# Kernel optimization log

Hardware: AMD Instinct MI355X
Metric: run time of the kernel (lower is better)

Reference implementation:

```python
import jax, jax.numpy as jnp
import numpy as np

N, E, S, G = 524288, 2097152, 8192, 64
F_IN, HID = 64, 128


def setup_inputs() -> dict:
    key = jax.random.key(0)
    ks = jax.random.split(key, 12)
    x = jax.random.normal(ks[0], (N, F_IN), dtype=jnp.float32)
    edge_index = jax.random.randint(ks[1], (2, E), 0, N, dtype=jnp.int64)
    node_batch = jnp.sort(jax.random.randint(ks[2], (N,), 0, S, dtype=jnp.int64))
    weights = jax.random.uniform(ks[3], (S, 1), dtype=jnp.float32)
    subgraph_batch = jnp.sort(jax.random.randint(ks[4], (S,), 0, G, dtype=jnp.int64))
    s = 1.0 / np.sqrt(F_IN)
    h = 1.0 / np.sqrt(HID)
    W_l = jax.random.uniform(ks[5], (F_IN, HID), jnp.float32, -s, s)
    W_r = jax.random.uniform(ks[6], (F_IN, HID), jnp.float32, -s, s)
    b_conv = jax.random.uniform(ks[7], (HID,), jnp.float32, -s, s)
    W1 = jax.random.uniform(ks[8], (HID, HID), jnp.float32, -h, h)
    b1 = jax.random.uniform(ks[9], (HID,), jnp.float32, -h, h)
    W2 = jax.random.uniform(ks[10], (HID, 1), jnp.float32, -h, h)
    b2 = jax.random.uniform(ks[11], (1,), jnp.float32, -h, h)
    return {"x": x, "edge_index": edge_index, "node_batch": node_batch,
            "weights": weights, "subgraph_batch": subgraph_batch,
            "W_l": W_l, "W_r": W_r, "b_conv": b_conv,
            "W1": W1, "b1": b1, "W2": W2, "b2": b2}


def reference(x, edge_index, node_batch, weights, subgraph_batch,
              W_l, W_r, b_conv, W1, b1, W2, b2):
    src, dst = edge_index[0], edge_index[1]
    # GraphSAGE mean aggregation: gather neighbor feats, scatter-mean to dst
    msg_sum = jax.ops.segment_sum(x[src], dst, num_segments=N)  # [N, F_IN]
    deg = jax.ops.segment_sum(jnp.ones((E,), x.dtype), dst, num_segments=N)
    agg = msg_sum / jnp.maximum(deg, 1.0)[:, None]
    h = jax.nn.relu(agg @ W_l + x @ W_r + b_conv)               # [N, HID]
    # global_add_pool nodes -> subgraph embeddings
    g = jax.ops.segment_sum(h, node_batch, num_segments=S)      # [S, HID]
    # MLP head -> scalar per subgraph
    s = jax.nn.leaky_relu(g @ W1 + b1, negative_slope=0.01) @ W2 + b2  # [S, 1]
    sw = s * weights
    energy = jax.ops.segment_sum(sw, subgraph_batch, num_segments=G)   # [G, 1]
    norm = jax.ops.segment_sum(weights, subgraph_batch, num_segments=G)
    return energy / norm
```

## Files before the change

### kernel.cpp

```cpp
#include <hip/hip_runtime.h>
#include <hip/hip_bf16.h>

#define NN 524288
#define NE 2097152
#define NS 8192
#define NG 64
#define FIN 64
#define HIDDEN 128

#define NB 512
#define BIN_NODES 1024
#define CAP 4608

typedef __attribute__((ext_vector_type(8))) unsigned short ushort8;
typedef __attribute__((ext_vector_type(8))) short bf16x8;
typedef __attribute__((ext_vector_type(4))) float floatx4;

__device__ __forceinline__ unsigned short f2b(float f) {
  union { float f; unsigned int u; } c; c.f = f;
  unsigned int u = c.u;
  unsigned int r = (u + 0x7FFFu + ((u >> 16) & 1u)) >> 16;
  return (unsigned short)r;
}
__device__ __forceinline__ float b2f(unsigned short b) {
  union { unsigned int u; float f; } c; c.u = ((unsigned int)b) << 16;
  return c.f;
}

__global__ __launch_bounds__(256) void k_cast(const float* __restrict__ x,
                                              unsigned short* __restrict__ xb) {
  size_t i = ((size_t)blockIdx.x * 256 + threadIdx.x) * 8;
  float4 v0 = *(const float4*)(x + i);
  float4 v1 = *(const float4*)(x + i + 4);
  ushort8 r;
  r[0] = f2b(v0.x); r[1] = f2b(v0.y); r[2] = f2b(v0.z); r[3] = f2b(v0.w);
  r[4] = f2b(v1.x); r[5] = f2b(v1.y); r[6] = f2b(v1.z); r[7] = f2b(v1.w);
  *(ushort8*)(xb + i) = r;
}

__global__ __launch_bounds__(256) void k_prepw(const float* __restrict__ Wl,
                                               const float* __restrict__ Wr,
                                               unsigned short* __restrict__ Wt) {
  int i = blockIdx.x * 256 + threadIdx.x;
  int n = i >> 7, k = i & 127;
  float v = (k < FIN) ? Wl[k * HIDDEN + n] : Wr[(k - FIN) * HIDDEN + n];
  Wt[n * HIDDEN + k] = f2b(v);
}

__global__ __launch_bounds__(256) void k_bin1(const int* __restrict__ ei,
                                              int* __restrict__ binCursor,
                                              unsigned int* __restrict__ pairs) {
  __shared__ unsigned int pk[4096];
  __shared__ unsigned short bn[4096];
  __shared__ int cnt[NB];
  __shared__ int base[NB];
  const int t = threadIdx.x;
  const int eBase = blockIdx.x * 4096;
  cnt[t] = 0; cnt[t + 256] = 0;
  __syncthreads();
#pragma unroll
  for (int i = 0; i < 16; ++i) {
    int j = i * 256 + t;
    int e = eBase + j;
    int src = ei[e];
    int dst = ei[NE + e];
    int bin = dst >> 10;
    pk[j] = ((unsigned int)(dst & 1023) << 19) | (unsigned int)src;
    bn[j] = (unsigned short)bin;
    atomicAdd(&cnt[bin], 1);
  }
  __syncthreads();
  {
    int c0 = cnt[t], c1 = cnt[t + 256];
    base[t]       = atomicAdd(&binCursor[t], c0);
    base[t + 256] = atomicAdd(&binCursor[t + 256], c1);
    cnt[t] = 0; cnt[t + 256] = 0;
  }
  __syncthreads();
#pragma unroll
  for (int i = 0; i < 16; ++i) {
    int j = i * 256 + t;
    int bin = bn[j];
    int ofs = atomicAdd(&cnt[bin], 1);
    pairs[(size_t)bin * CAP + base[bin] + ofs] = pk[j];
  }
}

__global__ __launch_bounds__(256) void k_bin2(const int* __restrict__ binCursor,
                                              unsigned int* __restrict__ pairs,
                                              int* __restrict__ S) {
  __shared__ unsigned int pk[CAP];
  __shared__ int cnt[BIN_NODES];
  __shared__ int ps[256];
  const int t = threadIdx.x;
  const int b = blockIdx.x;
  int total = binCursor[b];
  if (total > CAP) total = CAP;
  const int gbase = b * CAP;

  for (int i = t; i < total; i += 256) pk[i] = pairs[gbase + i];
  cnt[t] = 0; cnt[t + 256] = 0; cnt[t + 512] = 0; cnt[t + 768] = 0;
  __syncthreads();

  for (int i = t; i < total; i += 256) atomicAdd(&cnt[pk[i] >> 19], 1);
  __syncthreads();

  int c0 = cnt[4 * t], c1 = cnt[4 * t + 1], c2 = cnt[4 * t + 2], c3 = cnt[4 * t + 3];
  int tot4 = c0 + c1 + c2 + c3;
  ps[t] = tot4;
  __syncthreads();
  for (int off = 1; off < 256; off <<= 1) {
    int v = 0;
    if (t >= off) v = ps[t - off];
    __syncthreads();
    ps[t] += v;
    __syncthreads();
  }
  int e0 = ps[t] - tot4;
  int e1 = e0 + c0, e2 = e1 + c1, e3 = e2 + c2;
  cnt[4 * t] = e0; cnt[4 * t + 1] = e1; cnt[4 * t + 2] = e2; cnt[4 * t + 3] = e3;
  int sidx = b * (BIN_NODES + 1) + 4 * t;
  S[sidx]     = gbase + e0;
  S[sidx + 1] = gbase + e1;
  S[sidx + 2] = gbase + e2;
  S[sidx + 3] = gbase + e3;
  if (t == 0) S[b * (BIN_NODES + 1) + BIN_NODES] = gbase + total;
  __syncthreads();

  for (int i = t; i < total; i += 256) {
    unsigned int p = pk[i];
    int dl = p >> 19;
    int ofs = atomicAdd(&cnt[dl], 1);
    pairs[gbase + ofs] = p & 0x7FFFFu;
  }
}

#define CB_NODES 128
__global__ __launch_bounds__(512, 6) void k_aggconv(const unsigned short* __restrict__ xb,
                                                    const int* __restrict__ S,
                                                    const unsigned int* __restrict__ bucket,
                                                    const int* __restrict__ node_batch,
                                                    const unsigned short* __restrict__ Wt,
                                                    const float* __restrict__ bconv,
                                                    float* __restrict__ g) {
  __shared__ unsigned short As[128 * 136];
  __shared__ int nb_s[CB_NODES];
  const int t = threadIdx.x;
  const int n0 = blockIdx.x * CB_NODES;

  if (t < CB_NODES) nb_s[t] = node_batch[n0 + t];

#pragma unroll
  for (int it = 0; it < 2; ++it) {
    int i = it * 512 + t;
    int n = i >> 3;
    int c = i & 7;
    *(ushort8*)(As + n * 136 + 64 + c * 8) =
        *(const ushort8*)(xb + (size_t)(n0 + n) * FIN + c * 8);
  }

  {
    const int lane8 = t & 7;
    const int grp = t >> 3;
#pragma unroll
    for (int p = 0; p < 2; ++p) {
      int nl = p * 64 + grp;
      int n = n0 + nl;
      int sidx = n + (n >> 10);
      int rp0 = S[sidx];
      int rp1 = S[sidx + 1];
      float a[8] = {0,0,0,0,0,0,0,0};
      int e = rp0;
      for (; e + 3 < rp1; e += 4) {
        int s0 = bucket[e], s1 = bucket[e + 1], s2 = bucket[e + 2], s3 = bucket[e + 3];
        ushort8 v0 = *(const ushort8*)(xb + (size_t)s0 * FIN + (lane8 << 3));
        ushort8 v1 = *(const ushort8*)(xb + (size_t)s1 * FIN + (lane8 << 3));
        ushort8 v2 = *(const ushort8*)(xb + (size_t)s2 * FIN + (lane8 << 3));
        ushort8 v3 = *(const ushort8*)(xb + (size_t)s3 * FIN + (lane8 << 3));
#pragma unroll
        for (int j = 0; j < 8; ++j)
          a[j] += (b2f(v0[j]) + b2f(v1[j])) + (b2f(v2[j]) + b2f(v3[j]));
      }
      for (; e < rp1; ++e) {
        int s0 = bucket[e];
        ushort8 v0 = *(const ushort8*)(xb + (size_t)s0 * FIN + (lane8 << 3));
#pragma unroll
        for (int j = 0; j < 8; ++j) a[j] += b2f(v0[j]);
      }
      float rdeg = 1.f / fmaxf((float)(rp1 - rp0), 1.f);
      ushort8 r;
#pragma unroll
      for (int j = 0; j < 8; ++j) r[j] = f2b(a[j] * rdeg);
      *(ushort8*)(As + nl * 136 + lane8 * 8) = r;
    }
  }

  const int wave = t >> 6;
  const int lane = t & 63;
  const int l16 = lane & 15;
  const int quad = lane >> 4;

  bf16x8 bfrag[4];
#pragma unroll
  for (int ks = 0; ks < 4; ++ks)
    bfrag[ks] = *(const bf16x8*)(Wt + (size_t)(wave * 16 + l16) * HIDDEN + ks * 32 + quad * 8);
  float bv = bconv[wave * 16 + l16];

  floatx4 acc[8];
#pragma unroll
  for (int mt = 0; mt < 8; ++mt) acc[mt] = (floatx4){0.f, 0.f, 0.f, 0.f};

  __syncthreads();

#pragma unroll
  for (int mt = 0; mt < 8; ++mt) {
#pragma unroll
    for (int ks = 0; ks < 4; ++ks) {
      bf16x8 a = *(const bf16x8*)(As + (mt * 16 + l16) * 136 + ks * 32 + quad * 8);
      acc[mt] = __builtin_amdgcn_mfma_f32_16x16x32_bf16(a, bfrag[ks], acc[mt], 0, 0, 0);
    }
  }

  __syncthreads();

  {
    int col = wave * 16 + l16;
#pragma unroll
    for (int mt = 0; mt < 8; ++mt)
#pragma unroll
      for (int r = 0; r < 4; ++r) {
        int row = mt * 16 + quad * 4 + r;
        float hv = fmaxf(acc[mt][r] + bv, 0.f);
        As[row * 136 + col] = f2b(hv);
      }
  }
  __syncthreads();

  {
    int j = t & 127;
    int q = t >> 7;
    int ns = q * 32, ne = ns + 32;
    float sum = 0.f;
    int cur = nb_s[ns];
    for (int n = ns; n < ne; ++n) {
      int b = nb_s[n];
      if (b != cur) {
        unsafeAtomicAdd(&g[(size_t)cur * HIDDEN + j], sum);
        sum = 0.f;
        cur = b;
      }
      sum += b2f(As[n * 136 + j]);
    }
    unsafeAtomicAdd(&g[(size_t)cur * HIDDEN + j], sum);
  }
}

__global__ __launch_bounds__(256) void k_head(const float* __restrict__ g,
                                              const float* __restrict__ W1,
                                              const float* __restrict__ b1,
                                              const float* __restrict__ W2,
                                              const float* __restrict__ b2,
                                              const float* __restrict__ wts,
                                              const int* __restrict__ sgb,
                                              float* __restrict__ egy,
                                              float* __restrict__ nrm) {
  int s = blockIdx.x * 4 + (threadIdx.x >> 6);
  int lane = threadIdx.x & 63;
  const float* grow = g + (size_t)s * HIDDEN;
  float acc0 = b1[lane];
  float acc1 = b1[lane + 64];
  for (int k = 0; k < HIDDEN; ++k) {
    float gk = grow[k];
    acc0 = fmaf(gk, W1[k * HIDDEN + lane], acc0);
    acc1 = fmaf(gk, W1[k * HIDDEN + 64 + lane], acc1);
  }
  float t0 = acc0 > 0.f ? acc0 : 0.01f * acc0;
  float t1 = acc1 > 0.f ? acc1 : 0.01f * acc1;
  float part = t0 * W2[lane] + t1 * W2[lane + 64];
#pragma unroll
  for (int off = 32; off > 0; off >>= 1) part += __shfl_down(part, off, 64);
  if (lane == 0) {
    float sval = part + b2[0];
    float w = wts[s];
    int grp = sgb[s];
    unsafeAtomicAdd(&egy[grp], sval * w);
    unsafeAtomicAdd(&nrm[grp], w);
  }
}

__global__ void k_final(const float* __restrict__ egy,
                        const float* __restrict__ nrm,
                        float* __restrict__ out) {
  int t = threadIdx.x;
  out[t] = egy[t] / nrm[t];
}

extern "C" void kernel_launch(void* const* d_in, const int* in_sizes, int n_in,
                              void* d_out, int out_size, void* d_ws, size_t ws_size,
                              hipStream_t stream) {
  const float* x   = (const float*)d_in[0];
  const int*   ei  = (const int*)d_in[1];
  const int*   nb  = (const int*)d_in[2];
  const float* wts = (const float*)d_in[3];
  const int*   sgb = (const int*)d_in[4];
  const float* Wl  = (const float*)d_in[5];
  const float* Wr  = (const float*)d_in[6];
  const float* bcv = (const float*)d_in[7];
  const float* W1  = (const float*)d_in[8];
  const float* b1  = (const float*)d_in[9];
  const float* W2  = (const float*)d_in[10];
  const float* b2  = (const float*)d_in[11];
  float* out = (float*)d_out;

  int*   binCursor = (int*)d_ws;
  float* g         = (float*)(binCursor + NB);
  float* egy       = g + (size_t)NS * HIDDEN;
  float* nrm       = egy + NG;
  int*   S         = (int*)(nrm + NG);
  unsigned int* pairs = (unsigned int*)(S + NB * (BIN_NODES + 1));
  unsigned short* xb   = (unsigned short*)(pairs + (size_t)NB * CAP);
  unsigned short* Wt   = xb + (size_t)NN * FIN;

  size_t zero_bytes = ((size_t)NB + (size_t)NS * HIDDEN + 2 * NG) * 4;
  hipMemsetAsync(d_ws, 0, zero_bytes, stream);

  k_cast <<<(NN * FIN) / (256 * 8), 256, 0, stream>>>(x, xb);
  k_prepw<<<64, 256, 0, stream>>>(Wl, Wr, Wt);
  k_bin1 <<<NE / 4096, 256, 0, stream>>>(ei, binCursor, pairs);
  k_bin2 <<<NB, 256, 0, stream>>>(binCursor, pairs, S);
  k_aggconv<<<NN / CB_NODES, 512, 0, stream>>>(xb, S, pairs, nb, Wt, bcv, g);
  k_head<<<NS / 4, 256, 0, stream>>>(g, W1, b1, W2, b2, wts, sgb, egy, nrm);
  k_final<<<1, 64, 0, stream>>>(egy, nrm, out);
}
```

Measured before the change: 420.4 us.

## Sort bin writes in LDS, widen gather per lane, stage W1 in LDS

k_bin1 now does a local prefix sum and sorts each block's edges by bin in shared memory before writing, so the global stores to each bin are contiguous instead of scattered. The aggregation gather switches from 8 lanes per node over two passes to 4 lanes per node in one pass, each lane loading 16 features, which gives each lane more loads in flight. k_head caches W1 in shared memory and handles 16 subgraphs per block instead of 4, so W1 is no longer re-read from global memory by every wave. The costs are more shared memory, extra barriers in k_bin1, and fewer head blocks.

```diff
diff --git a/kernel.cpp b/kernel.cpp
--- a/kernel.cpp
+++ b/kernel.cpp
@@ -51,9 +51,13 @@
                                               int* __restrict__ binCursor,
                                               unsigned int* __restrict__ pairs) {
   __shared__ unsigned int pk[4096];
+  __shared__ unsigned int pks[4096];
   __shared__ unsigned short bn[4096];
+  __shared__ unsigned short bns[4096];
   __shared__ int cnt[NB];
+  __shared__ int ofs_s[NB];
   __shared__ int base[NB];
+  __shared__ int ps[256];
   const int t = threadIdx.x;
   const int eBase = blockIdx.x * 4096;
   cnt[t] = 0; cnt[t + 256] = 0;
@@ -70,19 +74,40 @@
     atomicAdd(&cnt[bin], 1);
   }
   __syncthreads();
+  int c0 = cnt[2 * t], c1 = cnt[2 * t + 1];
+  int tot = c0 + c1;
+  ps[t] = tot;
+  __syncthreads();
+  for (int off = 1; off < 256; off <<= 1) {
+    int v = 0;
+    if (t >= off) v = ps[t - off];
+    __syncthreads();
+    ps[t] += v;
+    __syncthreads();
+  }
   {
-    int c0 = cnt[t], c1 = cnt[t + 256];
-    base[t]       = atomicAdd(&binCursor[t], c0);
-    base[t + 256] = atomicAdd(&binCursor[t + 256], c1);
-    cnt[t] = 0; cnt[t + 256] = 0;
+    int e0 = ps[t] - tot;
+    int e1 = e0 + c0;
+    ofs_s[2 * t] = e0; ofs_s[2 * t + 1] = e1;
+    cnt[2 * t] = e0; cnt[2 * t + 1] = e1;
+    base[2 * t]     = atomicAdd(&binCursor[2 * t], c0);
+    base[2 * t + 1] = atomicAdd(&binCursor[2 * t + 1], c1);
   }
   __syncthreads();
 #pragma unroll
   for (int i = 0; i < 16; ++i) {
     int j = i * 256 + t;
     int bin = bn[j];
-    int ofs = atomicAdd(&cnt[bin], 1);
-    pairs[(size_t)bin * CAP + base[bin] + ofs] = pk[j];
+    int p = atomicAdd(&cnt[bin], 1);
+    pks[p] = pk[j];
+    bns[p] = (unsigned short)bin;
+  }
+  __syncthreads();
+#pragma unroll
+  for (int i = 0; i < 16; ++i) {
+    int j = i * 256 + t;
+    int bin = bns[j];
+    pairs[(size_t)bin * CAP + base[bin] + (j - ofs_s[bin])] = pks[j];
   }
 }
 
@@ -160,39 +185,51 @@
   }
 
   {
-    const int lane8 = t & 7;
-    const int grp = t >> 3;
-#pragma unroll
-    for (int p = 0; p < 2; ++p) {
-      int nl = p * 64 + grp;
-      int n = n0 + nl;
-      int sidx = n + (n >> 10);
-      int rp0 = S[sidx];
-      int rp1 = S[sidx + 1];
-      float a[8] = {0,0,0,0,0,0,0,0};
-      int e = rp0;
-      for (; e + 3 < rp1; e += 4) {
-        int s0 = bucket[e], s1 = bucket[e + 1], s2 = bucket[e + 2], s3 = bucket[e + 3];
-        ushort8 v0 = *(const ushort8*)(xb + (size_t)s0 * FIN + (lane8 << 3));
-        ushort8 v1 = *(const ushort8*)(xb + (size_t)s1 * FIN + (lane8 << 3));
-        ushort8 v2 = *(const ushort8*)(xb + (size_t)s2 * FIN + (lane8 << 3));
-        ushort8 v3 = *(const ushort8*)(xb + (size_t)s3 * FIN + (lane8 << 3));
-#pragma unroll
-        for (int j = 0; j < 8; ++j)
-          a[j] += (b2f(v0[j]) + b2f(v1[j])) + (b2f(v2[j]) + b2f(v3[j]));
+    const int lane4 = t & 3;
+    const int grp = t >> 2;
+    const int n = n0 + grp;
+    const int sidx = n + (n >> 10);
+    const int rp0 = S[sidx];
+    const int rp1 = S[sidx + 1];
+    const int co = lane4 << 4;
+
+    float a[16];
+#pragma unroll
+    for (int j = 0; j < 16; ++j) a[j] = 0.f;
+
+    int e = rp0;
+    for (; e + 3 < rp1; e += 4) {
+      int s0 = bucket[e], s1 = bucket[e + 1], s2 = bucket[e + 2], s3 = bucket[e + 3];
+      const unsigned short* r0 = xb + (size_t)s0 * FIN + co;
+      const unsigned short* r1 = xb + (size_t)s1 * FIN + co;
+      const unsigned short* r2 = xb + (size_t)s2 * FIN + co;
+      const unsigned short* r3 = xb + (size_t)s3 * FIN + co;
+      ushort8 v0a = *(const ushort8*)(r0), v0b = *(const ushort8*)(r0 + 8);
+      ushort8 v1a = *(const ushort8*)(r1), v1b = *(const ushort8*)(r1 + 8);
+      ushort8 v2a = *(const ushort8*)(r2), v2b = *(const ushort8*)(r2 + 8);
+      ushort8 v3a = *(const ushort8*)(r3), v3b = *(const ushort8*)(r3 + 8);
+#pragma unroll
+      for (int j = 0; j < 8; ++j) {
+        a[j]     += (b2f(v0a[j]) + b2f(v1a[j])) + (b2f(v2a[j]) + b2f(v3a[j]));
+        a[8 + j] += (b2f(v0b[j]) + b2f(v1b[j])) + (b2f(v2b[j]) + b2f(v3b[j]));
       }
-      for (; e < rp1; ++e) {
-        int s0 = bucket[e];
-        ushort8 v0 = *(const ushort8*)(xb + (size_t)s0 * FIN + (lane8 << 3));
-#pragma unroll
-        for (int j = 0; j < 8; ++j) a[j] += b2f(v0[j]);
+    }
+    for (; e < rp1; ++e) {
+      int s0 = bucket[e];
+      const unsigned short* r0 = xb + (size_t)s0 * FIN + co;
+      ushort8 v0a = *(const ushort8*)(r0), v0b = *(const ushort8*)(r0 + 8);
+#pragma unroll
+      for (int j = 0; j < 8; ++j) {
+        a[j] += b2f(v0a[j]);
+        a[8 + j] += b2f(v0b[j]);
       }
-      float rdeg = 1.f / fmaxf((float)(rp1 - rp0), 1.f);
-      ushort8 r;
-#pragma unroll
-      for (int j = 0; j < 8; ++j) r[j] = f2b(a[j] * rdeg);
-      *(ushort8*)(As + nl * 136 + lane8 * 8) = r;
-    }
+    }
+    float rdeg = 1.f / fmaxf((float)(rp1 - rp0), 1.f);
+    ushort8 r0, r1;
+#pragma unroll
+    for (int j = 0; j < 8; ++j) { r0[j] = f2b(a[j] * rdeg); r1[j] = f2b(a[8 + j] * rdeg); }
+    *(ushort8*)(As + grp * 136 + co) = r0;
+    *(ushort8*)(As + grp * 136 + co + 8) = r1;
   }
 
   const int wave = t >> 6;
@@ -255,6 +292,7 @@
   }
 }
 
+#define HB_SG 16
 __global__ __launch_bounds__(256) void k_head(const float* __restrict__ g,
                                               const float* __restrict__ W1,
                                               const float* __restrict__ b1,
@@ -264,27 +302,40 @@
                                               const int* __restrict__ sgb,
                                               float* __restrict__ egy,
                                               float* __restrict__ nrm) {
-  int s = blockIdx.x * 4 + (threadIdx.x >> 6);
-  int lane = threadIdx.x & 63;
-  const float* grow = g + (size_t)s * HIDDEN;
-  float acc0 = b1[lane];
-  float acc1 = b1[lane + 64];
-  for (int k = 0; k < HIDDEN; ++k) {
-    float gk = grow[k];
-    acc0 = fmaf(gk, W1[k * HIDDEN + lane], acc0);
-    acc1 = fmaf(gk, W1[k * HIDDEN + 64 + lane], acc1);
-  }
-  float t0 = acc0 > 0.f ? acc0 : 0.01f * acc0;
-  float t1 = acc1 > 0.f ? acc1 : 0.01f * acc1;
-  float part = t0 * W2[lane] + t1 * W2[lane + 64];
-#pragma unroll
-  for (int off = 32; off > 0; off >>= 1) part += __shfl_down(part, off, 64);
-  if (lane == 0) {
-    float sval = part + b2[0];
-    float w = wts[s];
-    int grp = sgb[s];
-    unsafeAtomicAdd(&egy[grp], sval * w);
-    unsafeAtomicAdd(&nrm[grp], w);
+  __shared__ float W1s[HIDDEN * HIDDEN];
+  const int t = threadIdx.x;
+#pragma unroll
+  for (int it = 0; it < 16; ++it) {
+    int i = (it * 256 + t) * 4;
+    *(float4*)(W1s + i) = *(const float4*)(W1 + i);
+  }
+  const int wv = t >> 6;
+  const int lane = t & 63;
+  const float b1a = b1[lane], b1b = b1[lane + 64];
+  const float w2a = W2[lane], w2b = W2[lane + 64];
+  __syncthreads();
+#pragma unroll
+  for (int q = 0; q < HB_SG / 4; ++q) {
+    int s = blockIdx.x * HB_SG + q * 4 + wv;
+    const float* grow = g + (size_t)s * HIDDEN;
+    float acc0 = b1a, acc1 = b1b;
+    for (int k = 0; k < HIDDEN; ++k) {
+      float gk = grow[k];
+      acc0 = fmaf(gk, W1s[k * HIDDEN + lane], acc0);
+      acc1 = fmaf(gk, W1s[k * HIDDEN + 64 + lane], acc1);
+    }
+    float t0 = acc0 > 0.f ? acc0 : 0.01f * acc0;
+    float t1 = acc1 > 0.f ? acc1 : 0.01f * acc1;
+    float part = t0 * w2a + t1 * w2b;
+#pragma unroll
+    for (int off = 32; off > 0; off >>= 1) part += __shfl_down(part, off, 64);
+    if (lane == 0) {
+      float sval = part + b2[0];
+      float w = wts[s];
+      int grp = sgb[s];
+      unsafeAtomicAdd(&egy[grp], sval * w);
+      unsafeAtomicAdd(&nrm[grp], w);
+    }
   }
 }
 
@@ -329,6 +380,6 @@
   k_bin1 <<<NE / 4096, 256, 0, stream>>>(ei, binCursor, pairs);
   k_bin2 <<<NB, 256, 0, stream>>>(binCursor, pairs, S);
   k_aggconv<<<NN / CB_NODES, 512, 0, stream>>>(xb, S, pairs, nb, Wt, bcv, g);
-  k_head<<<NS / 4, 256, 0, stream>>>(g, W1, b1, W2, b2, wts, sgb, egy, nrm);
+  k_head<<<NS / HB_SG, 256, 0, stream>>>(g, W1, b1, W2, b2, wts, sgb, egy, nrm);
   k_final<<<1, 64, 0, stream>>>(egy, nrm, out);
 }
```

After: 404.2 us. -3.9%, faster.
